# Kernel optimization log

Measured on AMD Instinct MI355X. Metric: run time of the kernel, lower is better.

Reference implementation:

```python
import jax, jax.numpy as jnp
import numpy as np

B, T, V, E, H, C = 128, 512, 100000, 100, 128, 3


def _lstm_dir(xs, w_ih, w_hh, b, reverse=False):
    # xs: [T,B,D]; w_ih: [4H,D]; w_hh: [4H,H]; b: [4H] (b_ih+b_hh combined)
    Tn, Bn, _ = xs.shape
    Hn = w_hh.shape[1]
    if reverse:
        xs = xs[::-1]
    gx = jnp.einsum('tbd,gd->tbg', xs, w_ih) + b  # [T,B,4H] input projections

    def step(carry, g_in):
        h, c = carry
        gates = g_in + h @ w_hh.T
        i, f, g, o = jnp.split(gates, 4, axis=-1)  # torch gate order i,f,g,o
        i = jax.nn.sigmoid(i)
        f = jax.nn.sigmoid(f)
        g = jnp.tanh(g)
        o = jax.nn.sigmoid(o)
        c = f * c + i * g
        h = o * jnp.tanh(c)
        return (h, c), h

    init = (jnp.zeros((Bn, Hn), xs.dtype), jnp.zeros((Bn, Hn), xs.dtype))
    (h_last, _), hs = jax.lax.scan(step, init, gx)
    if reverse:
        hs = hs[::-1]
    return hs, h_last


def setup_inputs() -> dict:
    key = jax.random.key(0)
    ks = jax.random.split(key, 24)
    s_e = 1.0 / np.sqrt(H)

    def u(k, shape):
        return jax.random.uniform(k, shape, jnp.float32, -s_e, s_e)

    x = jax.random.randint(ks[0], (B, T), 0, V, dtype=jnp.int32)
    emb = jax.random.normal(ks[1], (V, E), jnp.float32)
    emb = emb.at[0].set(0.0)  # padding_idx=0
    inp = {'x': x, 'emb': emb}
    names = []
    idx = 2
    for layer, din in ((0, E), (1, 2 * H)):
        for suf in ('', 'r'):
            inp[f'w_ih_l{layer}{suf}'] = u(ks[idx], (4 * H, din)); idx += 1
            inp[f'w_hh_l{layer}{suf}'] = u(ks[idx], (4 * H, H)); idx += 1
            inp[f'b_ih_l{layer}{suf}'] = u(ks[idx], (4 * H,)); idx += 1
            inp[f'b_hh_l{layer}{suf}'] = u(ks[idx], (4 * H,)); idx += 1
    s_f = 1.0 / np.sqrt(2 * H)
    inp['fc_w'] = jax.random.uniform(ks[22], (C, 2 * H), jnp.float32, -s_f, s_f)
    inp['fc_b'] = jax.random.uniform(ks[23], (C,), jnp.float32, -s_f, s_f)
    return inp


def reference(x, emb, w_ih_l0, w_hh_l0, b_ih_l0, b_hh_l0,
              w_ih_l0r, w_hh_l0r, b_ih_l0r, b_hh_l0r,
              w_ih_l1, w_hh_l1, b_ih_l1, b_hh_l1,
              w_ih_l1r, w_hh_l1r, b_ih_l1r, b_hh_l1r,
              fc_w, fc_b):
    # dropout is identity in eval mode
    xe = emb[x]                      # [B,T,E]
    xs = jnp.transpose(xe, (1, 0, 2))  # [T,B,E]
    # layer 0 bidirectional
    hf0, _ = _lstm_dir(xs, w_ih_l0, w_hh_l0, b_ih_l0 + b_hh_l0, reverse=False)
    hb0, _ = _lstm_dir(xs, w_ih_l0r, w_hh_l0r, b_ih_l0r + b_hh_l0r, reverse=True)
    x1 = jnp.concatenate([hf0, hb0], axis=-1)  # [T,B,2H]
    # layer 1 bidirectional; only final hidden states needed
    _, hF = _lstm_dir(x1, w_ih_l1, w_hh_l1, b_ih_l1 + b_hh_l1, reverse=False)
    _, hB = _lstm_dir(x1, w_ih_l1r, w_hh_l1r, b_ih_l1r + b_hh_l1r, reverse=True)
    out = jnp.concatenate([hF, hB], axis=1)  # [B,2H] == cat(hidden[-2], hidden[-1])
    return out @ fc_w.T + fc_b  # [B,C]
```

## Files before the change

kernel.cpp:

```cpp
#include <hip/hip_runtime.h>
#include <hip/hip_bf16.h>
#include <math.h>

#define TT 512
#define BB 128
#define EE 100
#define HH 128
#define G4 512
#define K1 256

typedef __attribute__((ext_vector_type(8))) short bf16x8;
typedef __attribute__((ext_vector_type(4))) float f32x4;

__device__ inline unsigned short bf16_rne(float v) {
    __hip_bfloat16 h = __float2bfloat16(v);
    return *reinterpret_cast<unsigned short*>(&h);
}

__device__ inline void gload16(const void* g, void* l) {
    __builtin_amdgcn_global_load_lds(
        (const __attribute__((address_space(1))) void*)g,
        (__attribute__((address_space(3))) void*)l, 16, 0, 0);
}

template<int CTRL>
__device__ inline float dppf(float x) {
    int r = __builtin_amdgcn_update_dpp(0, __float_as_int(x), CTRL, 0xF, 0xF, true);
    return __int_as_float(r);
}

__device__ inline float sig_fast(float z) {
    return __builtin_amdgcn_rcpf(1.f + __expf(-z));
}

__global__ void embed_cvt(const int* __restrict__ x, const float* __restrict__ emb,
                          unsigned short* __restrict__ xs2) {
    int row = blockIdx.x;
    int k = threadIdx.x;
    int b = row & 127, t = row >> 7;
    int tok = x[b * TT + t];
    float v = (k < EE) ? emb[(size_t)tok * EE + k] : 0.f;
    xs2[(size_t)row * 128 + k] = bf16_rne(v);
}

__global__ void wcvt2(const float* __restrict__ srcf, const float* __restrict__ srcr,
                      int Kin, int Kp,
                      unsigned short* __restrict__ dstf, unsigned short* __restrict__ dstr) {
    const float* src = blockIdx.y ? srcr : srcf;
    unsigned short* dst = blockIdx.y ? dstr : dstf;
    int n = blockIdx.x;
    int k = threadIdx.x;
    int j = n & 3;
    int gate = ((j & 1) << 1) | (j >> 1);
    int r = gate * 128 + (n >> 2);
    float v = (k < Kin) ? src[(size_t)r * Kin + k] : 0.f;
    dst[(size_t)n * Kp + k] = bf16_rne(v);
}

__global__ void bias2(const float* __restrict__ bihf0, const float* __restrict__ bhhf0,
                      const float* __restrict__ bihr0, const float* __restrict__ bhhr0,
                      const float* __restrict__ bihf1, const float* __restrict__ bhhf1,
                      const float* __restrict__ bihr1, const float* __restrict__ bhhr1,
                      float* __restrict__ dst) {
    int n = blockIdx.x * 256 + threadIdx.x;
    int layer = n >> 10;
    int d = (n >> 9) & 1, m = n & 511;
    int j = m & 3;
    int gate = ((j & 1) << 1) | (j >> 1);
    int src = gate * 128 + (m >> 2);
    const float* a = layer ? (d ? bihr1 : bihf1) : (d ? bihr0 : bihf0);
    const float* c = layer ? (d ? bhhr1 : bhhf1) : (d ? bhhr0 : bhhf0);
    dst[n] = a[src] + c[src];
}

__global__ void whh_pack4(const float* __restrict__ w0f, const float* __restrict__ w0r,
                          const float* __restrict__ w1f, const float* __restrict__ w1r,
                          float* __restrict__ dstbase) {
    int which = blockIdx.y;
    const float* src = which == 0 ? w0f : which == 1 ? w0r : which == 2 ? w1f : w1r;
    float* dst = dstbase + (size_t)which * 128 * 128 * 4;
    int u = blockIdx.x;
    int k = threadIdx.x;
    float4 v;
    v.x = src[((size_t)(0 * 128 + u)) * 128 + k];
    v.y = src[((size_t)(1 * 128 + u)) * 128 + k];
    v.z = src[((size_t)(2 * 128 + u)) * 128 + k];
    v.w = src[((size_t)(3 * 128 + u)) * 128 + k];
    reinterpret_cast<float4*>(dst)[(size_t)u * 128 + k] = v;
}

template<int K2>
__global__ __launch_bounds__(256) void gemm_mfma(
    const unsigned short* __restrict__ A2,
    const unsigned short* __restrict__ W2cat,
    const float* __restrict__ biascat,
    float* __restrict__ Cf, float* __restrict__ Cr,
    int t_base)
{
    __shared__ bf16x8 As[1024];
    __shared__ bf16x8 Bs[1024];
    int tid = threadIdx.x;
    int s = blockIdx.y;
    int dir = blockIdx.x >> 2;
    int nBase = (blockIdx.x & 3) * 128;
    int t = dir ? (TT - 1 - t_base - s) : (t_base + s);
    float* C = dir ? Cr : Cf;
    const unsigned short* Abase = A2 + (size_t)t * BB * K2;
    const unsigned short* Wbase = W2cat + (size_t)(dir * 512 + nBase) * K2;
    int lane = tid & 63, wid = tid >> 6;
    int wr = wid >> 1, wc = wid & 1;
    int l15 = lane & 15, g = lane >> 4;

    f32x4 acc[4][4];
    const f32x4 z = {0.f, 0.f, 0.f, 0.f};
    #pragma unroll
    for (int i = 0; i < 4; ++i)
        #pragma unroll
        for (int j = 0; j < 4; ++j) acc[i][j] = z;

    for (int kt = 0; kt < K2 / 64; ++kt) {
        #pragma unroll
        for (int j = 0; j < 4; ++j) {
            int p = tid + j * 256;
            int row = p >> 3;
            int k16 = (p & 7) ^ (row & 7);
            size_t goff = (size_t)row * K2 + kt * 64 + k16 * 8;
            gload16(Abase + goff, &As[p]);
            gload16(Wbase + goff, &Bs[p]);
        }
        __syncthreads();
        #pragma unroll
        for (int ks = 0; ks < 2; ++ks) {
            bf16x8 af[4], bfr[4];
            #pragma unroll
            for (int i = 0; i < 4; ++i) {
                int arow = wr * 64 + i * 16 + l15;
                int abyte = arow * 128 + ((ks * 64 + g * 16) ^ ((arow & 7) << 4));
                af[i] = As[abyte >> 4];
                int brow = wc * 64 + i * 16 + l15;
                int bbyte = brow * 128 + ((ks * 64 + g * 16) ^ ((brow & 7) << 4));
                bfr[i] = Bs[bbyte >> 4];
            }
            #pragma unroll
            for (int i = 0; i < 4; ++i)
                #pragma unroll
                for (int j = 0; j < 4; ++j)
                    acc[i][j] = __builtin_amdgcn_mfma_f32_16x16x32_bf16(
                        af[i], bfr[j], acc[i][j], 0, 0, 0);
        }
        __syncthreads();
    }
    int l3 = l15 & 3;
    int cquad = l15 & 12;
    bool lb0 = (l15 & 1) != 0;
    bool lb1 = (l15 & 2) != 0;
    #pragma unroll
    for (int i = 0; i < 4; ++i) {
        int row = s * 128 + wr * 64 + i * 16 + g * 4 + l3;
        float* Crow = C + (size_t)row * G4;
        #pragma unroll
        for (int j = 0; j < 4; ++j) {
            int colb = nBase + wc * 64 + j * 16 + cquad;
            float4 bv = *reinterpret_cast<const float4*>(&biascat[dir * 512 + colb]);
            f32x4 v = acc[i][j];
            float t0 = dppf<0xB1>(v[1]);
            float t1 = dppf<0xB1>(v[0]);
            float t2 = dppf<0xB1>(v[3]);
            float t3 = dppf<0xB1>(v[2]);
            float T0 = lb0 ? t0 : v[0];
            float T1 = lb0 ? v[1] : t1;
            float T2 = lb0 ? t2 : v[2];
            float T3 = lb0 ? v[3] : t3;
            float s0 = dppf<0x4E>(T2);
            float s1 = dppf<0x4E>(T3);
            float s2 = dppf<0x4E>(T0);
            float s3 = dppf<0x4E>(T1);
            float W0 = lb1 ? s0 : T0;
            float W1 = lb1 ? s1 : T1;
            float W2 = lb1 ? T2 : s2;
            float W3 = lb1 ? T3 : s3;
            float4 outv = {W0 + bv.x, W1 + bv.y, W2 + bv.z, W3 + bv.w};
            *reinterpret_cast<float4*>(&Crow[colb]) = outv;
        }
    }
}

__global__ __launch_bounds__(512, 2) void lstm_chunk(
    const float* __restrict__ gxf,
    const float* __restrict__ gxr,
    const float* __restrict__ wpkf,
    const float* __restrict__ wpkr,
    float* __restrict__ h_state,
    float* __restrict__ c_state,
    unsigned short* __restrict__ out_x1,
    int t_base, int TC, int init)
{
    int blk = blockIdx.x;
    int dir = blk >> 7;
    int b   = blk & 127;
    const float* gx  = dir ? gxr : gxf;
    const float* wpk = dir ? wpkr : wpkf;
    int tid = threadIdx.x;
    int u = tid >> 2, q = tid & 3;

    const f32x4* wp4 = reinterpret_cast<const f32x4*>(wpk) + ((size_t)u * 128 + q * 32);
#define LW(i) const f32x4 w##i = wp4[i];
    LW(0)  LW(1)  LW(2)  LW(3)  LW(4)  LW(5)  LW(6)  LW(7)
    LW(8)  LW(9)  LW(10) LW(11) LW(12) LW(13) LW(14) LW(15)
    LW(16) LW(17) LW(18) LW(19) LW(20) LW(21) LW(22) LW(23)
    LW(24) LW(25) LW(26) LW(27) LW(28) LW(29) LW(30) LW(31)
#undef LW

    __shared__ float hb[2][160];
    int sbase = (dir * BB + b) * HH;
    int hslot = (u >> 5) * 40 + (u & 31);
    float c = init ? 0.f : c_state[sbase + u];
    float h = init ? 0.f : h_state[sbase + u];
    if (q == 0) hb[0][hslot] = h;
    __syncthreads();

    const size_t SSTR = (size_t)BB * G4;
    const float* gxrow = gx + b * G4 + tid;
    bool odd2 = (q & 2) != 0;
    bool oddq = (q & 1) != 0;
    float fq = (q == 1) ? 2.f : 1.f;
    float bq = (q == 1) ? -1.f : 0.f;

    float g0 = gxrow[0 * SSTR];
    float g1 = gxrow[1 * SSTR];
    float g2 = gxrow[2 * SSTR];
    float g3 = gxrow[3 * SSTR];

#define STEPB(J, GIN) { \
        constexpr int p2 = (J) & 1; \
        const float4* hb4 = reinterpret_cast<const float4*>(&hb[p2][40 * q]); \
        float4 hv0 = hb4[0], hv1 = hb4[1], hv2 = hb4[2], hv3 = hb4[3]; \
        float4 hv4 = hb4[4], hv5 = hb4[5], hv6 = hb4[6], hv7 = hb4[7]; \
        f32x4 a0 = {0.f,0.f,0.f,0.f}, a1 = {0.f,0.f,0.f,0.f}; \
        f32x4 a2 = {0.f,0.f,0.f,0.f}, a3 = {0.f,0.f,0.f,0.f}; \
        FM(0,1,2,3,hv0)    FM(4,5,6,7,hv1)    FM(8,9,10,11,hv2)  FM(12,13,14,15,hv3) \
        FM(16,17,18,19,hv4) FM(20,21,22,23,hv5) FM(24,25,26,27,hv6) FM(28,29,30,31,hv7) \
        f32x4 acc = (a0 + a1) + (a2 + a3); \
        float xs = acc.x + dppf<0xB1>(acc.x); \
        float ys = acc.y + dppf<0xB1>(acc.y); \
        float zs = acc.z + dppf<0xB1>(acc.z); \
        float ws = acc.w + dppf<0xB1>(acc.w); \
        float sa = oddq ? zs : xs; \
        float sb = oddq ? ws : ys; \
        float sa2 = sa + dppf<0x4E>(sa); \
        float sb2 = sb + dppf<0x4E>(sb); \
        float pre_dot = odd2 ? sb2 : sa2; \
        float pre = pre_dot + (GIN); \
        float act = __builtin_fmaf(sig_fast(pre * fq), fq, bq); \
        float ig = dppf<0x00>(act); \
        float gg = dppf<0x55>(act); \
        float fg = dppf<0xAA>(act); \
        float og = dppf<0xFF>(act); \
        c = fg * c + ig * gg; \
        float th = __builtin_fmaf(2.f, sig_fast(2.f * c), -1.f); \
        h = og * th; \
        if (q == 0) { \
            hb[p2 ^ 1][hslot] = h; \
            if (out_x1) { \
                int sg = t_base + s + (J); \
                int tg = dir ? (TT - 1 - sg) : sg; \
                out_x1[((size_t)tg * BB + b) * 256 + dir * HH + u] = bf16_rne(h); \
            } \
        } \
        asm volatile("s_waitcnt lgkmcnt(0)" ::: "memory"); \
        __builtin_amdgcn_s_barrier(); \
        asm volatile("" ::: "memory"); \
    }
#define FM(i0,i1,i2,i3,HV) { \
        f32x4 hh; \
        hh = f32x4{HV.x,HV.x,HV.x,HV.x}; a0 = __builtin_elementwise_fma(w##i0, hh, a0); \
        hh = f32x4{HV.y,HV.y,HV.y,HV.y}; a1 = __builtin_elementwise_fma(w##i1, hh, a1); \
        hh = f32x4{HV.z,HV.z,HV.z,HV.z}; a2 = __builtin_elementwise_fma(w##i2, hh, a2); \
        hh = f32x4{HV.w,HV.w,HV.w,HV.w}; a3 = __builtin_elementwise_fma(w##i3, hh, a3); }

    for (int s = 0; s < TC; s += 4) {
        int nbase = (s + 4 <= TC - 4) ? (s + 4) : (TC - 4);
        float n0 = gxrow[(size_t)(nbase + 0) * SSTR];
        float n1 = gxrow[(size_t)(nbase + 1) * SSTR];
        float n2 = gxrow[(size_t)(nbase + 2) * SSTR];
        float n3 = gxrow[(size_t)(nbase + 3) * SSTR];
        STEPB(0, g0)
        STEPB(1, g1)
        STEPB(2, g2)
        STEPB(3, g3)
        g0 = n0; g1 = n1; g2 = n2; g3 = n3;
    }
#undef FM
#undef STEPB

    if (q == 0) {
        h_state[sbase + u] = h;
        c_state[sbase + u] = c;
    }
}

__global__ void fc_kernel(const float* __restrict__ h_state,
                          const float* __restrict__ fc_w,
                          const float* __restrict__ fc_b,
                          float* __restrict__ out) {
    int tid = blockIdx.x * blockDim.x + threadIdx.x;
    if (tid >= BB * 3) return;
    int b = tid / 3;
    int c = tid % 3;
    float acc = 0.f;
    for (int j = 0; j < 256; ++j) {
        float v = (j < HH) ? h_state[((size_t)0 * BB + b) * HH + j]
                           : h_state[((size_t)1 * BB + b) * HH + (j - HH)];
        acc += v * fc_w[c * 256 + j];
    }
    out[b * 3 + c] = acc + fc_b[c];
}

extern "C" void kernel_launch(void* const* d_in, const int* in_sizes, int n_in,
                              void* d_out, int out_size, void* d_ws, size_t ws_size,
                              hipStream_t stream) {
    const int*   x        = (const int*)  d_in[0];
    const float* emb      = (const float*)d_in[1];
    const float* w_ih_l0  = (const float*)d_in[2];
    const float* w_hh_l0  = (const float*)d_in[3];
    const float* b_ih_l0  = (const float*)d_in[4];
    const float* b_hh_l0  = (const float*)d_in[5];
    const float* w_ih_l0r = (const float*)d_in[6];
    const float* w_hh_l0r = (const float*)d_in[7];
    const float* b_ih_l0r = (const float*)d_in[8];
    const float* b_hh_l0r = (const float*)d_in[9];
    const float* w_ih_l1  = (const float*)d_in[10];
    const float* w_hh_l1  = (const float*)d_in[11];
    const float* b_ih_l1  = (const float*)d_in[12];
    const float* b_hh_l1  = (const float*)d_in[13];
    const float* w_ih_l1r = (const float*)d_in[14];
    const float* w_hh_l1r = (const float*)d_in[15];
    const float* b_ih_l1r = (const float*)d_in[16];
    const float* b_hh_l1r = (const float*)d_in[17];
    const float* fc_w     = (const float*)d_in[18];
    const float* fc_b     = (const float*)d_in[19];
    float* out = (float*)d_out;
    (void)in_sizes; (void)n_in; (void)out_size;

    size_t xs2_b   = (size_t)TT * BB * 128 * 2;
    size_t x1_b    = (size_t)TT * BB * 256 * 2;
    size_t w2l0_b  = (size_t)512 * 128 * 2;
    size_t w2l1_b  = (size_t)512 * 256 * 2;
    size_t bias_b  = (size_t)1024 * 4;
    size_t wpk_b   = (size_t)128 * 128 * 4 * 4;
    size_t state_b = (size_t)2 * BB * HH * 4;
    size_t fixed = xs2_b + x1_b + 2 * w2l0_b + 2 * w2l1_b + 2 * bias_b
                 + 4 * wpk_b + 2 * state_b + 4096;
    int TC = 256;
    while (TC > 8) {
        size_t chunk2 = (size_t)TC * BB * G4 * 4 * 2;
        if (fixed + chunk2 <= ws_size) break;
        TC >>= 1;
    }
    char* ws = (char*)d_ws;
    size_t off = 0;
    unsigned short* xs2   = (unsigned short*)(ws + off); off += xs2_b;
    unsigned short* x1_2  = (unsigned short*)(ws + off); off += x1_b;
    unsigned short* w2l0f = (unsigned short*)(ws + off); off += w2l0_b;
    unsigned short* w2l0r = (unsigned short*)(ws + off); off += w2l0_b;
    unsigned short* w2l1f = (unsigned short*)(ws + off); off += w2l1_b;
    unsigned short* w2l1r = (unsigned short*)(ws + off); off += w2l1_b;
    float* biasl0  = (float*)(ws + off); off += bias_b;
    float* biasl1  = (float*)(ws + off); off += bias_b;
    float* wpk0f   = (float*)(ws + off); off += wpk_b;
    float* wpk0r   = (float*)(ws + off); off += wpk_b;
    float* wpk1f   = (float*)(ws + off); off += wpk_b;
    float* wpk1r   = (float*)(ws + off); off += wpk_b;
    float* h_state = (float*)(ws + off); off += state_b;
    float* c_state = (float*)(ws + off); off += state_b;
    float* gxf     = (float*)(ws + off); off += (size_t)TC * BB * G4 * 4;
    float* gxr     = (float*)(ws + off);

    int NC = TT / TC;

    embed_cvt<<<TT * BB, 128, 0, stream>>>(x, emb, xs2);
    wcvt2<<<dim3(512, 2), 128, 0, stream>>>(w_ih_l0, w_ih_l0r, EE, 128, w2l0f, w2l0r);
    wcvt2<<<dim3(512, 2), 256, 0, stream>>>(w_ih_l1, w_ih_l1r, K1, 256, w2l1f, w2l1r);
    bias2<<<8, 256, 0, stream>>>(b_ih_l0, b_hh_l0, b_ih_l0r, b_hh_l0r,
                                 b_ih_l1, b_hh_l1, b_ih_l1r, b_hh_l1r, biasl0);
    whh_pack4<<<dim3(128, 4), 128, 0, stream>>>(w_hh_l0, w_hh_l0r, w_hh_l1, w_hh_l1r, wpk0f);

    for (int ci = 0; ci < NC; ++ci) {
        int t0 = ci * TC;
        gemm_mfma<128><<<dim3(8, TC), 256, 0, stream>>>(xs2, w2l0f, biasl0, gxf, gxr, t0);
        lstm_chunk<<<256, 512, 0, stream>>>(gxf, gxr, wpk0f, wpk0r,
                                            h_state, c_state, x1_2, t0, TC, ci == 0);
    }
    for (int ci = 0; ci < NC; ++ci) {
        int t0 = ci * TC;
        gemm_mfma<256><<<dim3(8, TC), 256, 0, stream>>>(x1_2, w2l1f, biasl1, gxf, gxr, t0);
        lstm_chunk<<<256, 512, 0, stream>>>(gxf, gxr, wpk1f, wpk1r,
                                            h_state, c_state, nullptr, t0, TC, ci == 0);
    }
    fc_kernel<<<2, 192, 0, stream>>>(h_state, fc_w, fc_b, out);
}
```

Before: 795.2 us.

## Split LSTM recurrent dot product across 8 lanes per hidden unit

The recurrent step kernel now uses 1024 threads per block, with 8 lanes per hidden unit instead of 4. Each lane holds half as many weight registers and runs half as many FMAs per step, and an extra cross-lane DPP reduction stage combines the partial sums. The aim is to shorten the serial per-step dependency chain and free registers. In exchange the block is larger, more lanes take part in each barrier, and the reduction adds one more step.

```diff
diff --git a/kernel.cpp b/kernel.cpp
--- a/kernel.cpp
+++ b/kernel.cpp
@@ -185,7 +185,7 @@
     }
 }
 
-__global__ __launch_bounds__(512, 2) void lstm_chunk(
+__global__ __launch_bounds__(1024, 1) void lstm_chunk(
     const float* __restrict__ gxf,
     const float* __restrict__ gxr,
     const float* __restrict__ wpkf,
@@ -201,14 +201,12 @@
     const float* gx  = dir ? gxr : gxf;
     const float* wpk = dir ? wpkr : wpkf;
     int tid = threadIdx.x;
-    int u = tid >> 2, q = tid & 3;
-
-    const f32x4* wp4 = reinterpret_cast<const f32x4*>(wpk) + ((size_t)u * 128 + q * 32);
+    int u = tid >> 3, o = tid & 7;
+
+    const f32x4* wp4 = reinterpret_cast<const f32x4*>(wpk) + ((size_t)u * 128 + o * 16);
 #define LW(i) const f32x4 w##i = wp4[i];
     LW(0)  LW(1)  LW(2)  LW(3)  LW(4)  LW(5)  LW(6)  LW(7)
     LW(8)  LW(9)  LW(10) LW(11) LW(12) LW(13) LW(14) LW(15)
-    LW(16) LW(17) LW(18) LW(19) LW(20) LW(21) LW(22) LW(23)
-    LW(24) LW(25) LW(26) LW(27) LW(28) LW(29) LW(30) LW(31)
 #undef LW
 
     __shared__ float hb[2][160];
@@ -216,40 +214,47 @@
     int hslot = (u >> 5) * 40 + (u & 31);
     float c = init ? 0.f : c_state[sbase + u];
     float h = init ? 0.f : h_state[sbase + u];
-    if (q == 0) hb[0][hslot] = h;
+    if (o == 0) hb[0][hslot] = h;
     __syncthreads();
 
+    int roff = (o >> 1) * 40 + (o & 1) * 16;
     const size_t SSTR = (size_t)BB * G4;
-    const float* gxrow = gx + b * G4 + tid;
-    bool odd2 = (q & 2) != 0;
-    bool oddq = (q & 1) != 0;
-    float fq = (q == 1) ? 2.f : 1.f;
-    float bq = (q == 1) ? -1.f : 0.f;
+    const float* gxrow = gx + b * G4 + 4 * u + (o & 3);
+    bool odd1 = (o & 1) != 0;
+    bool odd2 = (o & 2) != 0;
+    float fq = ((o & 3) == 1) ? 2.f : 1.f;
+    float bq = ((o & 3) == 1) ? -1.f : 0.f;
 
     float g0 = gxrow[0 * SSTR];
     float g1 = gxrow[1 * SSTR];
     float g2 = gxrow[2 * SSTR];
     float g3 = gxrow[3 * SSTR];
 
+#define FMA1(W, HV, A) A = __builtin_elementwise_fma(W, f32x4{HV, HV, HV, HV}, A)
 #define STEPB(J, GIN) { \
         constexpr int p2 = (J) & 1; \
-        const float4* hb4 = reinterpret_cast<const float4*>(&hb[p2][40 * q]); \
-        float4 hv0 = hb4[0], hv1 = hb4[1], hv2 = hb4[2], hv3 = hb4[3]; \
-        float4 hv4 = hb4[4], hv5 = hb4[5], hv6 = hb4[6], hv7 = hb4[7]; \
+        const float4* hp = reinterpret_cast<const float4*>(&hb[p2][roff]); \
+        float4 hA = hp[0], hB = hp[1], hC = hp[2], hD = hp[3]; \
         f32x4 a0 = {0.f,0.f,0.f,0.f}, a1 = {0.f,0.f,0.f,0.f}; \
-        f32x4 a2 = {0.f,0.f,0.f,0.f}, a3 = {0.f,0.f,0.f,0.f}; \
-        FM(0,1,2,3,hv0)    FM(4,5,6,7,hv1)    FM(8,9,10,11,hv2)  FM(12,13,14,15,hv3) \
-        FM(16,17,18,19,hv4) FM(20,21,22,23,hv5) FM(24,25,26,27,hv6) FM(28,29,30,31,hv7) \
-        f32x4 acc = (a0 + a1) + (a2 + a3); \
+        FMA1(w0,  hA.x, a0); FMA1(w1,  hA.y, a1); \
+        FMA1(w2,  hA.z, a0); FMA1(w3,  hA.w, a1); \
+        FMA1(w4,  hB.x, a0); FMA1(w5,  hB.y, a1); \
+        FMA1(w6,  hB.z, a0); FMA1(w7,  hB.w, a1); \
+        FMA1(w8,  hC.x, a0); FMA1(w9,  hC.y, a1); \
+        FMA1(w10, hC.z, a0); FMA1(w11, hC.w, a1); \
+        FMA1(w12, hD.x, a0); FMA1(w13, hD.y, a1); \
+        FMA1(w14, hD.z, a0); FMA1(w15, hD.w, a1); \
+        f32x4 acc = a0 + a1; \
         float xs = acc.x + dppf<0xB1>(acc.x); \
         float ys = acc.y + dppf<0xB1>(acc.y); \
         float zs = acc.z + dppf<0xB1>(acc.z); \
         float ws = acc.w + dppf<0xB1>(acc.w); \
-        float sa = oddq ? zs : xs; \
-        float sb = oddq ? ws : ys; \
+        float sa = odd1 ? zs : xs; \
+        float sb = odd1 ? ws : ys; \
         float sa2 = sa + dppf<0x4E>(sa); \
         float sb2 = sb + dppf<0x4E>(sb); \
-        float pre_dot = odd2 ? sb2 : sa2; \
+        float pd = odd2 ? sb2 : sa2; \
+        float pre_dot = pd + dppf<0x1B>(dppf<0x141>(pd)); \
         float pre = pre_dot + (GIN); \
         float act = __builtin_fmaf(sig_fast(pre * fq), fq, bq); \
         float ig = dppf<0x00>(act); \
@@ -259,7 +264,7 @@
         c = fg * c + ig * gg; \
         float th = __builtin_fmaf(2.f, sig_fast(2.f * c), -1.f); \
         h = og * th; \
-        if (q == 0) { \
+        if (o == 0) { \
             hb[p2 ^ 1][hslot] = h; \
             if (out_x1) { \
                 int sg = t_base + s + (J); \
@@ -271,12 +276,6 @@
         __builtin_amdgcn_s_barrier(); \
         asm volatile("" ::: "memory"); \
     }
-#define FM(i0,i1,i2,i3,HV) { \
-        f32x4 hh; \
-        hh = f32x4{HV.x,HV.x,HV.x,HV.x}; a0 = __builtin_elementwise_fma(w##i0, hh, a0); \
-        hh = f32x4{HV.y,HV.y,HV.y,HV.y}; a1 = __builtin_elementwise_fma(w##i1, hh, a1); \
-        hh = f32x4{HV.z,HV.z,HV.z,HV.z}; a2 = __builtin_elementwise_fma(w##i2, hh, a2); \
-        hh = f32x4{HV.w,HV.w,HV.w,HV.w}; a3 = __builtin_elementwise_fma(w##i3, hh, a3); }
 
     for (int s = 0; s < TC; s += 4) {
         int nbase = (s + 4 <= TC - 4) ? (s + 4) : (TC - 4);
@@ -290,10 +289,10 @@
         STEPB(3, g3)
         g0 = n0; g1 = n1; g2 = n2; g3 = n3;
     }
-#undef FM
 #undef STEPB
-
-    if (q == 0) {
+#undef FMA1
+
+    if (o == 0) {
         h_state[sbase + u] = h;
         c_state[sbase + u] = c;
     }
@@ -388,14 +387,14 @@
     for (int ci = 0; ci < NC; ++ci) {
         int t0 = ci * TC;
         gemm_mfma<128><<<dim3(8, TC), 256, 0, stream>>>(xs2, w2l0f, biasl0, gxf, gxr, t0);
-        lstm_chunk<<<256, 512, 0, stream>>>(gxf, gxr, wpk0f, wpk0r,
-                                            h_state, c_state, x1_2, t0, TC, ci == 0);
+        lstm_chunk<<<256, 1024, 0, stream>>>(gxf, gxr, wpk0f, wpk0r,
+                                             h_state, c_state, x1_2, t0, TC, ci == 0);
     }
     for (int ci = 0; ci < NC; ++ci) {
         int t0 = ci * TC;
         gemm_mfma<256><<<dim3(8, TC), 256, 0, stream>>>(x1_2, w2l1f, biasl1, gxf, gxr, t0);
-        lstm_chunk<<<256, 512, 0, stream>>>(gxf, gxr, wpk1f, wpk1r,
-                                            h_state, c_state, nullptr, t0, TC, ci == 0);
+        lstm_chunk<<<256, 1024, 0, stream>>>(gxf, gxr, wpk1f, wpk1r,
+                                             h_state, c_state, nullptr, t0, TC, ci == 0);
     }
     fc_kernel<<<2, 192, 0, stream>>>(h_state, fc_w, fc_b, out);
 }
```

Result: slower. 903.0 us (+13.5%).

## Store input-gate projections as fp16 and run each layer in one pass

Applied to the files above, without the earlier changes.

The input-projection GEMM now writes its gate pre-activations as fp16 instead of fp32, which halves the gx buffer, and the recurrence kernel converts them back to float on load. With the smaller buffer the whole sequence fits in the workspace, so the time-chunk loop goes away: one GEMM and one recurrence launch per layer, with state starting from zero inside the kernel. The launch bound drops to one block per CU. The risks are fp16 rounding and range limits on the gate inputs, and the workspace size is no longer checked against ws_size.

```diff
diff --git a/kernel.cpp b/kernel.cpp
--- a/kernel.cpp
+++ b/kernel.cpp
@@ -11,6 +11,7 @@
 
 typedef __attribute__((ext_vector_type(8))) short bf16x8;
 typedef __attribute__((ext_vector_type(4))) float f32x4;
+typedef __attribute__((ext_vector_type(4))) _Float16 f16x4;
 
 __device__ inline unsigned short bf16_rne(float v) {
     __hip_bfloat16 h = __float2bfloat16(v);
@@ -94,8 +95,7 @@
     const unsigned short* __restrict__ A2,
     const unsigned short* __restrict__ W2cat,
     const float* __restrict__ biascat,
-    float* __restrict__ Cf, float* __restrict__ Cr,
-    int t_base)
+    _Float16* __restrict__ Cf, _Float16* __restrict__ Cr)
 {
     __shared__ bf16x8 As[1024];
     __shared__ bf16x8 Bs[1024];
@@ -103,8 +103,8 @@
     int s = blockIdx.y;
     int dir = blockIdx.x >> 2;
     int nBase = (blockIdx.x & 3) * 128;
-    int t = dir ? (TT - 1 - t_base - s) : (t_base + s);
-    float* C = dir ? Cr : Cf;
+    int t = dir ? (TT - 1 - s) : s;
+    _Float16* C = dir ? Cr : Cf;
     const unsigned short* Abase = A2 + (size_t)t * BB * K2;
     const unsigned short* Wbase = W2cat + (size_t)(dir * 512 + nBase) * K2;
     int lane = tid & 63, wid = tid >> 6;
@@ -157,7 +157,7 @@
     #pragma unroll
     for (int i = 0; i < 4; ++i) {
         int row = s * 128 + wr * 64 + i * 16 + g * 4 + l3;
-        float* Crow = C + (size_t)row * G4;
+        _Float16* Crow = C + (size_t)row * G4;
         #pragma unroll
         for (int j = 0; j < 4; ++j) {
             int colb = nBase + wc * 64 + j * 16 + cquad;
@@ -179,26 +179,27 @@
             float W1 = lb1 ? s1 : T1;
             float W2 = lb1 ? T2 : s2;
             float W3 = lb1 ? T3 : s3;
-            float4 outv = {W0 + bv.x, W1 + bv.y, W2 + bv.z, W3 + bv.w};
-            *reinterpret_cast<float4*>(&Crow[colb]) = outv;
+            f16x4 outv = { (_Float16)(W0 + bv.x), (_Float16)(W1 + bv.y),
+                           (_Float16)(W2 + bv.z), (_Float16)(W3 + bv.w) };
+            *reinterpret_cast<f16x4*>(&Crow[colb]) = outv;
         }
     }
 }
 
-__global__ __launch_bounds__(512, 2) void lstm_chunk(
-    const float* __restrict__ gxf,
-    const float* __restrict__ gxr,
+__global__ __launch_bounds__(512, 1) void lstm_chunk(
+    const _Float16* __restrict__ gxf,
+    const _Float16* __restrict__ gxr,
     const float* __restrict__ wpkf,
     const float* __restrict__ wpkr,
     float* __restrict__ h_state,
     float* __restrict__ c_state,
     unsigned short* __restrict__ out_x1,
-    int t_base, int TC, int init)
+    float* __restrict__ hlast)
 {
     int blk = blockIdx.x;
     int dir = blk >> 7;
     int b   = blk & 127;
-    const float* gx  = dir ? gxr : gxf;
+    const _Float16* gx = dir ? gxr : gxf;
     const float* wpk = dir ? wpkr : wpkf;
     int tid = threadIdx.x;
     int u = tid >> 2, q = tid & 3;
@@ -214,22 +215,22 @@
     __shared__ float hb[2][160];
     int sbase = (dir * BB + b) * HH;
     int hslot = (u >> 5) * 40 + (u & 31);
-    float c = init ? 0.f : c_state[sbase + u];
-    float h = init ? 0.f : h_state[sbase + u];
-    if (q == 0) hb[0][hslot] = h;
+    float c = 0.f;
+    float h = 0.f;
+    if (q == 0) hb[0][hslot] = 0.f;
     __syncthreads();
 
     const size_t SSTR = (size_t)BB * G4;
-    const float* gxrow = gx + b * G4 + tid;
+    const _Float16* gxrow = gx + b * G4 + tid;
     bool odd2 = (q & 2) != 0;
     bool oddq = (q & 1) != 0;
     float fq = (q == 1) ? 2.f : 1.f;
     float bq = (q == 1) ? -1.f : 0.f;
 
-    float g0 = gxrow[0 * SSTR];
-    float g1 = gxrow[1 * SSTR];
-    float g2 = gxrow[2 * SSTR];
-    float g3 = gxrow[3 * SSTR];
+    float g0 = (float)gxrow[0 * SSTR];
+    float g1 = (float)gxrow[1 * SSTR];
+    float g2 = (float)gxrow[2 * SSTR];
+    float g3 = (float)gxrow[3 * SSTR];
 
 #define STEPB(J, GIN) { \
         constexpr int p2 = (J) & 1; \
@@ -262,7 +263,7 @@
         if (q == 0) { \
             hb[p2 ^ 1][hslot] = h; \
             if (out_x1) { \
-                int sg = t_base + s + (J); \
+                int sg = s + (J); \
                 int tg = dir ? (TT - 1 - sg) : sg; \
                 out_x1[((size_t)tg * BB + b) * 256 + dir * HH + u] = bf16_rne(h); \
             } \
@@ -278,12 +279,12 @@
         hh = f32x4{HV.z,HV.z,HV.z,HV.z}; a2 = __builtin_elementwise_fma(w##i2, hh, a2); \
         hh = f32x4{HV.w,HV.w,HV.w,HV.w}; a3 = __builtin_elementwise_fma(w##i3, hh, a3); }
 
-    for (int s = 0; s < TC; s += 4) {
-        int nbase = (s + 4 <= TC - 4) ? (s + 4) : (TC - 4);
-        float n0 = gxrow[(size_t)(nbase + 0) * SSTR];
-        float n1 = gxrow[(size_t)(nbase + 1) * SSTR];
-        float n2 = gxrow[(size_t)(nbase + 2) * SSTR];
-        float n3 = gxrow[(size_t)(nbase + 3) * SSTR];
+    for (int s = 0; s < TT; s += 4) {
+        int nbase = (s + 4 <= TT - 4) ? (s + 4) : (TT - 4);
+        float n0 = (float)gxrow[(size_t)(nbase + 0) * SSTR];
+        float n1 = (float)gxrow[(size_t)(nbase + 1) * SSTR];
+        float n2 = (float)gxrow[(size_t)(nbase + 2) * SSTR];
+        float n3 = (float)gxrow[(size_t)(nbase + 3) * SSTR];
         STEPB(0, g0)
         STEPB(1, g1)
         STEPB(2, g2)
@@ -294,6 +295,7 @@
 #undef STEPB
 
     if (q == 0) {
+        if (hlast) hlast[sbase + u] = h;
         h_state[sbase + u] = h;
         c_state[sbase + u] = c;
     }
@@ -340,7 +342,7 @@
     const float* fc_w     = (const float*)d_in[18];
     const float* fc_b     = (const float*)d_in[19];
     float* out = (float*)d_out;
-    (void)in_sizes; (void)n_in; (void)out_size;
+    (void)in_sizes; (void)n_in; (void)out_size; (void)ws_size;
 
     size_t xs2_b   = (size_t)TT * BB * 128 * 2;
     size_t x1_b    = (size_t)TT * BB * 256 * 2;
@@ -349,14 +351,7 @@
     size_t bias_b  = (size_t)1024 * 4;
     size_t wpk_b   = (size_t)128 * 128 * 4 * 4;
     size_t state_b = (size_t)2 * BB * HH * 4;
-    size_t fixed = xs2_b + x1_b + 2 * w2l0_b + 2 * w2l1_b + 2 * bias_b
-                 + 4 * wpk_b + 2 * state_b + 4096;
-    int TC = 256;
-    while (TC > 8) {
-        size_t chunk2 = (size_t)TC * BB * G4 * 4 * 2;
-        if (fixed + chunk2 <= ws_size) break;
-        TC >>= 1;
-    }
+    size_t gx_b    = (size_t)TT * BB * G4 * 2;
     char* ws = (char*)d_ws;
     size_t off = 0;
     unsigned short* xs2   = (unsigned short*)(ws + off); off += xs2_b;
@@ -373,10 +368,8 @@
     float* wpk1r   = (float*)(ws + off); off += wpk_b;
     float* h_state = (float*)(ws + off); off += state_b;
     float* c_state = (float*)(ws + off); off += state_b;
-    float* gxf     = (float*)(ws + off); off += (size_t)TC * BB * G4 * 4;
-    float* gxr     = (float*)(ws + off);
-
-    int NC = TT / TC;
+    _Float16* gxf  = (_Float16*)(ws + off); off += gx_b;
+    _Float16* gxr  = (_Float16*)(ws + off); off += gx_b;
 
     embed_cvt<<<TT * BB, 128, 0, stream>>>(x, emb, xs2);
     wcvt2<<<dim3(512, 2), 128, 0, stream>>>(w_ih_l0, w_ih_l0r, EE, 128, w2l0f, w2l0r);
@@ -385,17 +378,11 @@
                                  b_ih_l1, b_hh_l1, b_ih_l1r, b_hh_l1r, biasl0);
     whh_pack4<<<dim3(128, 4), 128, 0, stream>>>(w_hh_l0, w_hh_l0r, w_hh_l1, w_hh_l1r, wpk0f);
 
-    for (int ci = 0; ci < NC; ++ci) {
-        int t0 = ci * TC;
-        gemm_mfma<128><<<dim3(8, TC), 256, 0, stream>>>(xs2, w2l0f, biasl0, gxf, gxr, t0);
-        lstm_chunk<<<256, 512, 0, stream>>>(gxf, gxr, wpk0f, wpk0r,
-                                            h_state, c_state, x1_2, t0, TC, ci == 0);
-    }
-    for (int ci = 0; ci < NC; ++ci) {
-        int t0 = ci * TC;
-        gemm_mfma<256><<<dim3(8, TC), 256, 0, stream>>>(x1_2, w2l1f, biasl1, gxf, gxr, t0);
-        lstm_chunk<<<256, 512, 0, stream>>>(gxf, gxr, wpk1f, wpk1r,
-                                            h_state, c_state, nullptr, t0, TC, ci == 0);
-    }
+    gemm_mfma<128><<<dim3(8, TT), 256, 0, stream>>>(xs2, w2l0f, biasl0, gxf, gxr);
+    lstm_chunk<<<256, 512, 0, stream>>>(gxf, gxr, wpk0f, wpk0r,
+                                        h_state, c_state, x1_2, nullptr);
+    gemm_mfma<256><<<dim3(8, TT), 256, 0, stream>>>(x1_2, w2l1f, biasl1, gxf, gxr);
+    lstm_chunk<<<256, 512, 0, stream>>>(gxf, gxr, wpk1f, wpk1r,
+                                        h_state, c_state, nullptr, h_state);
     fc_kernel<<<2, 192, 0, stream>>>(h_state, fc_w, fc_b, out);
 }
```

Result: faster. 755.3 us (median of 2 runs) (-5.0%).
